# Kernel optimization log

Measured on AMD Instinct MI355X. Metric: run time of the kernel, lower is better.

## Reference

```python
import math
import jax, jax.numpy as jnp
import numpy as np

CAPACITY_FACTOR = 1.0
MIN_CAPACITY = 8


def setup_inputs() -> dict:
    key = jax.random.key(0)
    k1, k2 = jax.random.split(key)
    s, d, e = 8192, 1024, 64
    inputs = jax.random.normal(k1, (s, d), dtype=jnp.float32)
    wg_weight = jax.random.normal(k2, (e, d), dtype=jnp.float32) * (1.0 / math.sqrt(d))
    return {"inputs": inputs, "wg_weight": wg_weight}


def reference(inputs, wg_weight):
    # gate projection (always fp32 in the original)
    logits = inputs.astype(jnp.float32) @ wg_weight.T  # [s, e]
    s, e = logits.shape
    # static capacity: ceil(s/e * capacity_factor), floored at min_capacity
    capacity = max(int(math.ceil(s / e * CAPACITY_FACTOR)), MIN_CAPACITY)

    gates = jax.nn.softmax(logits, axis=1)            # [s, e]
    indices = jnp.argmax(gates, axis=1)               # [s]
    mask = jax.nn.one_hot(indices, e, dtype=jnp.int32)  # [s, e]
    exp_counts = jnp.sum(mask, axis=0)                # [e]

    # load-balancing aux loss (uses mask BEFORE capacity dropping)
    me = jnp.mean(gates, axis=0)
    ce = jnp.mean(mask.astype(jnp.float32), axis=0)
    l_aux = jnp.sum(me * ce) * e

    # capacity dropping: with use_rts=False, topk over the binary mask keeps
    # the first `capacity` tokens routed to each expert, i.e. cumulative
    # position-in-expert < capacity
    positions = jnp.cumsum(mask, axis=0) - 1          # [s, e]
    mask = mask * (positions < capacity).astype(jnp.int32)

    locations = jnp.cumsum(mask, axis=0) - 1          # [s, e]
    locations_s = jnp.sum(locations * mask, axis=1)   # [s] slot per token

    gates = gates * mask.astype(jnp.float32)          # zero out dropped tokens
    locations_sc = jax.nn.one_hot(locations_s, capacity, dtype=jnp.float32)  # [s, c]
    combine_weights = jnp.einsum('se,sc->sec', gates, locations_sc)  # [s, e, c]
    dispatch_mask = combine_weights.astype(bool)
    return l_aux, combine_weights, dispatch_mask, exp_counts
```

## Files before the change

kernel.cpp:

```cpp
#include <hip/hip_runtime.h>
#include <cstdint>
#include <cstddef>

#define S 8192
#define Dm 1024
#define E 64
#define CAP 128
#define SEC 67108864ull

#define GEMM_BLOCKS 256
#define FILL_BLOCKS 1792
#define N4ALL 33554448u

typedef float f32x4 __attribute__((ext_vector_type(4)));

__global__ __launch_bounds__(256) void k_main(const float* __restrict__ x,
                                              const float* __restrict__ w,
                                              float* __restrict__ gate,
                                              int* __restrict__ idx,
                                              float* __restrict__ me_part,
                                              float* __restrict__ out) {
    int bid = blockIdx.x;
    int tid = threadIdx.x;
    if (bid < GEMM_BLOCKS) {
        __shared__ float Al[32][68];
        __shared__ float Wl[64][68];
        __shared__ float sm[32];
        __shared__ float sinv[32];
        int rt = (tid & 15) * 2;
        int ce = (tid >> 4) * 4;
        int t0 = bid * 32;
        const float* asrc = x + (size_t)(t0 + (tid >> 3)) * Dm + (tid & 7) * 8;
        const float* wsrc0 = w + (size_t)(tid >> 3) * Dm + (tid & 7) * 8;
        const float* wsrc1 = wsrc0 + 32 * (size_t)Dm;
        float* adst = &Al[tid >> 3][(tid & 7) * 8];
        float* wdst0 = &Wl[tid >> 3][(tid & 7) * 8];
        float* wdst1 = &Wl[32 + (tid >> 3)][(tid & 7) * 8];

        float4 acc0 = make_float4(0.f, 0.f, 0.f, 0.f);
        float4 acc1 = make_float4(0.f, 0.f, 0.f, 0.f);

        float4 pa0 = *(const float4*)(asrc + 0);
        float4 pa1 = *(const float4*)(asrc + 4);
        float4 pw0 = *(const float4*)(wsrc0 + 0);
        float4 pw1 = *(const float4*)(wsrc0 + 4);
        float4 pw2 = *(const float4*)(wsrc1 + 0);
        float4 pw3 = *(const float4*)(wsrc1 + 4);
        float4 qa0 = *(const float4*)(asrc + 64);
        float4 qa1 = *(const float4*)(asrc + 68);
        float4 qw0 = *(const float4*)(wsrc0 + 64);
        float4 qw1 = *(const float4*)(wsrc0 + 68);
        float4 qw2 = *(const float4*)(wsrc1 + 64);
        float4 qw3 = *(const float4*)(wsrc1 + 68);

#define INNER_COMPUTE                                                          \
        _Pragma("unroll 4")                                                    \
        for (int k4 = 0; k4 < 16; ++k4) {                                      \
            float4 a0 = *(const float4*)&Al[rt][k4 * 4];                       \
            float4 a1 = *(const float4*)&Al[rt + 1][k4 * 4];                   \
            float4 w0 = *(const float4*)&Wl[ce + 0][k4 * 4];                   \
            float4 w1 = *(const float4*)&Wl[ce + 1][k4 * 4];                   \
            float4 w2 = *(const float4*)&Wl[ce + 2][k4 * 4];                   \
            float4 w3 = *(const float4*)&Wl[ce + 3][k4 * 4];                   \
            acc0.x = fmaf(a0.w, w0.w, fmaf(a0.z, w0.z, fmaf(a0.y, w0.y, fmaf(a0.x, w0.x, acc0.x)))); \
            acc0.y = fmaf(a0.w, w1.w, fmaf(a0.z, w1.z, fmaf(a0.y, w1.y, fmaf(a0.x, w1.x, acc0.y)))); \
            acc0.z = fmaf(a0.w, w2.w, fmaf(a0.z, w2.z, fmaf(a0.y, w2.y, fmaf(a0.x, w2.x, acc0.z)))); \
            acc0.w = fmaf(a0.w, w3.w, fmaf(a0.z, w3.z, fmaf(a0.y, w3.y, fmaf(a0.x, w3.x, acc0.w)))); \
            acc1.x = fmaf(a1.w, w0.w, fmaf(a1.z, w0.z, fmaf(a1.y, w0.y, fmaf(a1.x, w0.x, acc1.x)))); \
            acc1.y = fmaf(a1.w, w1.w, fmaf(a1.z, w1.z, fmaf(a1.y, w1.y, fmaf(a1.x, w1.x, acc1.y)))); \
            acc1.z = fmaf(a1.w, w2.w, fmaf(a1.z, w2.z, fmaf(a1.y, w2.y, fmaf(a1.x, w2.x, acc1.z)))); \
            acc1.w = fmaf(a1.w, w3.w, fmaf(a1.z, w3.z, fmaf(a1.y, w3.y, fmaf(a1.x, w3.x, acc1.w)))); \
        }

        for (int ch = 0; ch < 16; ch += 2) {
            __syncthreads();
            *(float4*)(adst + 0) = pa0;  *(float4*)(adst + 4) = pa1;
            *(float4*)(wdst0 + 0) = pw0; *(float4*)(wdst0 + 4) = pw1;
            *(float4*)(wdst1 + 0) = pw2; *(float4*)(wdst1 + 4) = pw3;
            __syncthreads();
            if (ch + 2 < 16) {
                int kb = (ch + 2) * 64;
                pa0 = *(const float4*)(asrc + kb);
                pa1 = *(const float4*)(asrc + kb + 4);
                pw0 = *(const float4*)(wsrc0 + kb);
                pw1 = *(const float4*)(wsrc0 + kb + 4);
                pw2 = *(const float4*)(wsrc1 + kb);
                pw3 = *(const float4*)(wsrc1 + kb + 4);
            }
            INNER_COMPUTE
            __syncthreads();
            *(float4*)(adst + 0) = qa0;  *(float4*)(adst + 4) = qa1;
            *(float4*)(wdst0 + 0) = qw0; *(float4*)(wdst0 + 4) = qw1;
            *(float4*)(wdst1 + 0) = qw2; *(float4*)(wdst1 + 4) = qw3;
            __syncthreads();
            if (ch + 3 < 16) {
                int kb = (ch + 3) * 64;
                qa0 = *(const float4*)(asrc + kb);
                qa1 = *(const float4*)(asrc + kb + 4);
                qw0 = *(const float4*)(wsrc0 + kb);
                qw1 = *(const float4*)(wsrc0 + kb + 4);
                qw2 = *(const float4*)(wsrc1 + kb);
                qw3 = *(const float4*)(wsrc1 + kb + 4);
            }
            INNER_COMPUTE
        }
#undef INNER_COMPUTE
        __syncthreads();
        Al[rt][ce + 0] = acc0.x; Al[rt][ce + 1] = acc0.y;
        Al[rt][ce + 2] = acc0.z; Al[rt][ce + 3] = acc0.w;
        Al[rt + 1][ce + 0] = acc1.x; Al[rt + 1][ce + 1] = acc1.y;
        Al[rt + 1][ce + 2] = acc1.z; Al[rt + 1][ce + 3] = acc1.w;
        __syncthreads();
        if (tid < 32) {
            float m = Al[tid][0];
            int am = 0;
#pragma unroll
            for (int c = 1; c < E; ++c) {
                float v = Al[tid][c];
                if (v > m) { m = v; am = c; }
            }
            float ssum = 0.f;
#pragma unroll
            for (int c = 0; c < E; ++c) ssum += __expf(Al[tid][c] - m);
            float inv = 1.0f / ssum;
            gate[t0 + tid] = inv;
            idx[t0 + tid] = am;
            sm[tid] = m;
            sinv[tid] = inv;
        }
        __syncthreads();
        if (tid < E) {
            float cs = 0.f;
#pragma unroll 8
            for (int r = 0; r < 32; ++r)
                cs += __expf(Al[r][tid] - sm[r]) * sinv[r];
            me_part[bid * E + tid] = cs;
        }
    } else {
        int fb = bid - GEMM_BLOCKS;
        f32x4 z = {0.f, 0.f, 0.f, 0.f};
        f32x4* o4 = (f32x4*)out;
        for (unsigned i = (unsigned)fb * 256u + tid; i < N4ALL;
             i += FILL_BLOCKS * 256u)
            o4[i] = z;
    }
}

__global__ __launch_bounds__(256) void k_scan(const int* __restrict__ idx,
                                              const float* __restrict__ gate,
                                              const float* __restrict__ me_part,
                                              float* __restrict__ out) {
    int e = blockIdx.x;
    int tid = threadIdx.x;
    int lane = tid & 63;
    int wid = tid >> 6;
    __shared__ int wsum[4];
    __shared__ float red[256];
    int running = 0;
    for (int ch = 0; ch < S / 256; ++ch) {
        int t = ch * 256 + tid;
        bool f = (idx[t] == e);
        unsigned long long b = __ballot(f);
        int pre = __popcll(b & ((1ull << lane) - 1ull));
        if (lane == 0) wsum[wid] = __popcll(b);
        __syncthreads();
        int off = running;
#pragma unroll
        for (int w2 = 0; w2 < 4; ++w2)
            if (w2 < wid) off += wsum[w2];
        int p = off + pre;
        if (f && p < CAP) {
            size_t o = 1 + (size_t)t * (E * CAP) + (size_t)e * CAP + (size_t)p;
            out[o] = gate[t];
            out[o + (size_t)SEC] = 1.0f;
        }
        running += wsum[0] + wsum[1] + wsum[2] + wsum[3];
        __syncthreads();
    }
    red[tid] = me_part[tid * E + e];
    __syncthreads();
    for (int s2 = 128; s2 > 0; s2 >>= 1) {
        if (tid < s2) red[tid] += red[tid + s2];
        __syncthreads();
    }
    if (tid == 0) {
        out[1 + 2 * (size_t)SEC + e] = (float)running;
        float la = red[0] * (1.0f / (float)S) *
                   ((float)running / (float)S) * (float)E;
        atomicAdd(out, la);
    }
}

extern "C" void kernel_launch(void* const* d_in, const int* in_sizes, int n_in,
                              void* d_out, int out_size, void* d_ws, size_t ws_size,
                              hipStream_t stream) {
    const float* x = (const float*)d_in[0];
    const float* w = (const float*)d_in[1];
    float* out = (float*)d_out;

    float* me_part = (float*)d_ws;
    float* gate = me_part + GEMM_BLOCKS * E;
    int* idx = (int*)(gate + S);

    k_main<<<dim3(GEMM_BLOCKS + FILL_BLOCKS), dim3(256), 0, stream>>>(
        x, w, gate, idx, me_part, out);
    k_scan<<<dim3(64), dim3(256), 0, stream>>>(idx, gate, me_part, out);
}
```

Baseline: 136.1 us.

## Split expert scan into token quarters using per-block expert counts

The GEMM blocks now also emit per-block counts of tokens routed to each expert. The scan kernel launches four blocks per expert, one per quarter of the tokens, and each seeds its running offset by reducing the counts of earlier blocks. This cuts the serial scan length fourfold and raises block count from 64 to 256. Separately, the zero-fill blocks now write contiguous chunks instead of grid-strided elements, which changes the memory access pattern of the large fill.

Measured after the change: 130.6 us. 4.1% less time.

```diff
diff --git a/kernel.cpp b/kernel.cpp
--- a/kernel.cpp
+++ b/kernel.cpp
@@ -11,6 +11,7 @@
 #define GEMM_BLOCKS 256
 #define FILL_BLOCKS 1792
 #define N4ALL 33554448u
+#define CHUNK4 18725u
 
 typedef float f32x4 __attribute__((ext_vector_type(4)));
 
@@ -19,6 +20,7 @@
                                               float* __restrict__ gate,
                                               int* __restrict__ idx,
                                               float* __restrict__ me_part,
+                                              int* __restrict__ cnt_g,
                                               float* __restrict__ out) {
     int bid = blockIdx.x;
     int tid = threadIdx.x;
@@ -27,6 +29,7 @@
         __shared__ float Wl[64][68];
         __shared__ float sm[32];
         __shared__ float sinv[32];
+        __shared__ int sidx[32];
         int rt = (tid & 15) * 2;
         int ce = (tid >> 4) * 4;
         int t0 = bid * 32;
@@ -127,38 +130,57 @@
             idx[t0 + tid] = am;
             sm[tid] = m;
             sinv[tid] = inv;
+            sidx[tid] = am;
         }
         __syncthreads();
         if (tid < E) {
             float cs = 0.f;
+            int cnt = 0;
 #pragma unroll 8
-            for (int r = 0; r < 32; ++r)
+            for (int r = 0; r < 32; ++r) {
                 cs += __expf(Al[r][tid] - sm[r]) * sinv[r];
+                cnt += (sidx[r] == tid) ? 1 : 0;
+            }
             me_part[bid * E + tid] = cs;
+            cnt_g[bid * E + tid] = cnt;
         }
     } else {
-        int fb = bid - GEMM_BLOCKS;
+        unsigned base4 = (unsigned)(bid - GEMM_BLOCKS) * CHUNK4;
         f32x4 z = {0.f, 0.f, 0.f, 0.f};
         f32x4* o4 = (f32x4*)out;
-        for (unsigned i = (unsigned)fb * 256u + tid; i < N4ALL;
-             i += FILL_BLOCKS * 256u)
-            o4[i] = z;
+        for (unsigned j = tid; j < CHUNK4; j += 256u) {
+            unsigned i = base4 + j;
+            if (i < N4ALL) o4[i] = z;
+        }
     }
 }
 
 __global__ __launch_bounds__(256) void k_scan(const int* __restrict__ idx,
                                               const float* __restrict__ gate,
                                               const float* __restrict__ me_part,
+                                              const int* __restrict__ cnt_g,
                                               float* __restrict__ out) {
-    int e = blockIdx.x;
+    int e = blockIdx.x >> 2;
+    int q = blockIdx.x & 3;
     int tid = threadIdx.x;
     int lane = tid & 63;
     int wid = tid >> 6;
     __shared__ int wsum[4];
+    __shared__ int ired[256];
     __shared__ float red[256];
-    int running = 0;
-    for (int ch = 0; ch < S / 256; ++ch) {
-        int t = ch * 256 + tid;
+    int nb = q << 6;
+    int a = 0;
+    for (int b = tid; b < nb; b += 256) a += cnt_g[b * E + e];
+    ired[tid] = a;
+    __syncthreads();
+    for (int s2 = 128; s2 > 0; s2 >>= 1) {
+        if (tid < s2) ired[tid] += ired[tid + s2];
+        __syncthreads();
+    }
+    int running = ired[0];
+    __syncthreads();
+    for (int ch = 0; ch < 8; ++ch) {
+        int t = q * 2048 + ch * 256 + tid;
         bool f = (idx[t] == e);
         unsigned long long b = __ballot(f);
         int pre = __popcll(b & ((1ull << lane) - 1ull));
@@ -177,17 +199,19 @@
         running += wsum[0] + wsum[1] + wsum[2] + wsum[3];
         __syncthreads();
     }
-    red[tid] = me_part[tid * E + e];
-    __syncthreads();
-    for (int s2 = 128; s2 > 0; s2 >>= 1) {
-        if (tid < s2) red[tid] += red[tid + s2];
-        __syncthreads();
-    }
-    if (tid == 0) {
-        out[1 + 2 * (size_t)SEC + e] = (float)running;
-        float la = red[0] * (1.0f / (float)S) *
-                   ((float)running / (float)S) * (float)E;
-        atomicAdd(out, la);
+    if (q == 3) {
+        red[tid] = me_part[tid * E + e];
+        __syncthreads();
+        for (int s2 = 128; s2 > 0; s2 >>= 1) {
+            if (tid < s2) red[tid] += red[tid + s2];
+            __syncthreads();
+        }
+        if (tid == 0) {
+            out[1 + 2 * (size_t)SEC + e] = (float)running;
+            float la = red[0] * (1.0f / (float)S) *
+                       ((float)running / (float)S) * (float)E;
+            atomicAdd(out, la);
+        }
     }
 }
 
@@ -201,8 +225,9 @@
     float* me_part = (float*)d_ws;
     float* gate = me_part + GEMM_BLOCKS * E;
     int* idx = (int*)(gate + S);
+    int* cnt_g = idx + S;
 
     k_main<<<dim3(GEMM_BLOCKS + FILL_BLOCKS), dim3(256), 0, stream>>>(
-        x, w, gate, idx, me_part, out);
-    k_scan<<<dim3(64), dim3(256), 0, stream>>>(idx, gate, me_part, out);
+        x, w, gate, idx, me_part, cnt_g, out);
+    k_scan<<<dim3(256), dim3(256), 0, stream>>>(idx, gate, me_part, cnt_g, out);
 }
```
